# Kernel tuning notes

Measured on AMD Instinct MI355X. Metric: run time of the kernel, lower is better.

## Reference

```python
import jax, jax.numpy as jnp
import numpy as np

H = 768          # hidden_size
NH = 12          # num heads
HD = H // NH     # head dim = 64
FF = 4 * H       # 3072
EPS = 1e-12


def _layer_norm(x, g, b):
    mu = jnp.mean(x, axis=-1, keepdims=True)
    var = jnp.var(x, axis=-1, keepdims=True)
    return (x - mu) * jax.lax.rsqrt(var + EPS) * g + b


def setup_inputs() -> dict:
    key = jax.random.key(0)
    ks = jax.random.split(key, 8)
    B, S = 4, 2048
    s = 0.02
    return {
        "x": jax.random.normal(ks[0], (B, S, H), dtype=jnp.float32),
        "w_qkv": jax.random.normal(ks[1], (H, 3 * H), dtype=jnp.float32) * s,
        "b_qkv": jnp.zeros((3 * H,), dtype=jnp.float32),
        "w_out": jax.random.normal(ks[2], (H, H), dtype=jnp.float32) * s,
        "b_out": jnp.zeros((H,), dtype=jnp.float32),
        "w_ff1": jax.random.normal(ks[3], (H, FF), dtype=jnp.float32) * s,
        "b_ff1": jnp.zeros((FF,), dtype=jnp.float32),
        "w_ff2": jax.random.normal(ks[4], (FF, H), dtype=jnp.float32) * s,
        "b_ff2": jnp.zeros((H,), dtype=jnp.float32),
        "g1": jnp.ones((H,), dtype=jnp.float32),
        "be1": jnp.zeros((H,), dtype=jnp.float32),
        "g2": jnp.ones((H,), dtype=jnp.float32),
        "be2": jnp.zeros((H,), dtype=jnp.float32),
    }


def reference(x, w_qkv, b_qkv, w_out, b_out, w_ff1, b_ff1, w_ff2, b_ff2, g1, be1, g2, be2):
    B, S, _ = x.shape
    qkv = x @ w_qkv + b_qkv                     # [B,S,3H]
    q, k, v = jnp.split(qkv, 3, axis=-1)
    # [B,S,H] -> [B,NH,S,HD]
    def heads(t):
        return t.reshape(B, S, NH, HD).transpose(0, 2, 1, 3)
    q, k, v = heads(q), heads(k), heads(v)
    scores = jnp.einsum("bhqd,bhkd->bhqk", q, k) / np.sqrt(HD).astype(np.float32)
    attn = jax.nn.softmax(scores, axis=-1)      # dropout is identity at inference
    ctx = jnp.einsum("bhqk,bhkd->bhqd", attn, v)
    ctx = ctx.transpose(0, 2, 1, 3).reshape(B, S, H)
    attn_out = ctx @ w_out + b_out
    x1 = _layer_norm(x + attn_out, g1, be1)
    h = jax.nn.gelu(x1 @ w_ff1 + b_ff1, approximate=False)  # torch exact gelu
    ffn = h @ w_ff2 + b_ff2
    return _layer_norm(x1 + ffn, g2, be2)
```

## Files before the change

### kernel.cpp

```cpp
#include <hip/hip_runtime.h>
#include <cstdint>
#include <cstddef>

typedef unsigned short u16;
typedef __attribute__((ext_vector_type(8))) short bf16x8;
typedef __attribute__((ext_vector_type(4))) float f32x4;
typedef __attribute__((ext_vector_type(16))) float f32x16;

__device__ __forceinline__ u16 f2b(float f) {
    union { float f; unsigned u; } un; un.f = f;
    unsigned r = un.u + 0x7fffu + ((un.u >> 16) & 1u);
    return (u16)(r >> 16);
}
__device__ __forceinline__ u16 f2b_trunc(float f) {
    union { float f; unsigned u; } un; un.f = f;
    return (u16)(un.u >> 16);
}
__device__ __forceinline__ float b2f(u16 h) {
    union { unsigned u; float f; } un; un.u = ((unsigned)h) << 16;
    return un.f;
}
__device__ __forceinline__ float fast_exp2(float x) {
#if __has_builtin(__builtin_amdgcn_exp2f)
    return __builtin_amdgcn_exp2f(x);
#else
    return exp2f(x);
#endif
}

__device__ __forceinline__ void stage16(const u16* g, u16* l) {
    __builtin_amdgcn_global_load_lds(
        (const __attribute__((address_space(1))) void*)g,
        (__attribute__((address_space(3))) void*)l, 16, 0, 0);
}

__global__ __launch_bounds__(256)
void prep(const float* __restrict__ x, u16* __restrict__ xb,
          const float* __restrict__ wqkv, u16* __restrict__ wqkvT,
          const float* __restrict__ wout, u16* __restrict__ woutT,
          const float* __restrict__ wff1, u16* __restrict__ wff1T,
          const float* __restrict__ wff2, u16* __restrict__ wff2T) {
    __shared__ float t[32][33];
    const int tid = threadIdx.x;
    int bid = blockIdx.x;
    if (bid < 6144) {
        const int i = bid * 256 + tid;
        float4 v = ((const float4*)x)[i];
        ushort4 o;
        o.x = f2b(v.x); o.y = f2b(v.y); o.z = f2b(v.z); o.w = f2b(v.w);
        ((ushort4*)xb)[i] = o;
        return;
    }
    int tt = bid - 6144;
    const float* in; u16* out; int K, N, bx, by;
    if (tt < 1728)      { in = wqkv; out = wqkvT; K = 768;  N = 2304; bx = tt % 72; by = tt / 72; }
    else if ((tt -= 1728) < 576)  { in = wout; out = woutT; K = 768;  N = 768;  bx = tt % 24; by = tt / 24; }
    else if ((tt -= 576) < 2304)  { in = wff1; out = wff1T; K = 768;  N = 3072; bx = tt % 96; by = tt / 96; }
    else { tt -= 2304;    in = wff2; out = wff2T; K = 3072; N = 768;  bx = tt % 24; by = tt / 24; }
    const int n0 = bx * 32, k0 = by * 32;
    const int tx = tid & 31, ty = tid >> 5;
#pragma unroll
    for (int i = 0; i < 4; ++i)
        t[ty + i * 8][tx] = in[(size_t)(k0 + ty + i * 8) * N + n0 + tx];
    __syncthreads();
#pragma unroll
    for (int i = 0; i < 4; ++i)
        out[(size_t)(n0 + ty + i * 8) * K + k0 + tx] = f2b(t[tx][ty + i * 8]);
}

template <int EPI>
__global__ __launch_bounds__(256, 3)
void gemm_bf16(const u16* __restrict__ A, const u16* __restrict__ BT,
               const float* __restrict__ bias,
               void* __restrict__ outp, u16* __restrict__ vt, int M, int N, int K) {
    __shared__ __align__(16) u16 Ash[128 * 64];
    __shared__ __align__(16) u16 Bsh[128 * 64];
    const int m0 = blockIdx.y * 128, n0 = blockIdx.x * 128;
    const int tid = threadIdx.x;
    const int w = tid >> 6, lane = tid & 63;
    const int l32 = lane & 31, half = lane >> 5;
    const int wm = (w >> 1) * 64, wn = (w & 1) * 64;

    const int srow = lane >> 3;
    const int sgrp = (lane & 7) ^ (srow & 7);
    const int xr = l32 & 7;

    f32x16 acc[2][2];
#pragma unroll
    for (int i = 0; i < 2; ++i)
#pragma unroll
        for (int j = 0; j < 2; ++j)
#pragma unroll
            for (int e = 0; e < 16; ++e) acc[i][j][e] = 0.f;

    for (int k0 = 0; k0 < K; k0 += 64) {
#pragma unroll
        for (int it = 0; it < 4; ++it) {
            const int c = it * 4 + w;
            const int r = c * 8 + srow;
            stage16(A + (size_t)(m0 + r) * K + k0 + sgrp * 8, &Ash[c * 512 + lane * 8]);
        }
#pragma unroll
        for (int it = 0; it < 4; ++it) {
            const int c = it * 4 + w;
            const int r = c * 8 + srow;
            stage16(BT + (size_t)(n0 + r) * K + k0 + sgrp * 8, &Bsh[c * 512 + lane * 8]);
        }
        __syncthreads();

        bf16x8 af[2][4], bfr[2][4];
#pragma unroll
        for (int mt = 0; mt < 2; ++mt)
#pragma unroll
            for (int kc = 0; kc < 4; ++kc)
                af[mt][kc] = *(const bf16x8*)&Ash[(wm + mt * 32 + l32) * 64 +
                                                  (((kc << 1) + half) ^ xr) * 8];
#pragma unroll
        for (int nt = 0; nt < 2; ++nt)
#pragma unroll
            for (int kc = 0; kc < 4; ++kc)
                bfr[nt][kc] = *(const bf16x8*)&Bsh[(wn + nt * 32 + l32) * 64 +
                                                   (((kc << 1) + half) ^ xr) * 8];
#pragma unroll
        for (int mt = 0; mt < 2; ++mt)
#pragma unroll
            for (int nt = 0; nt < 2; ++nt)
#pragma unroll
                for (int kc = 0; kc < 4; ++kc)
                    acc[mt][nt] = __builtin_amdgcn_mfma_f32_32x32x16_bf16(
                        af[mt][kc], bfr[nt][kc], acc[mt][nt], 0, 0, 0);
        __syncthreads();
    }

    if (EPI == 3 && n0 >= 1536) {
#pragma unroll
        for (int mt = 0; mt < 2; ++mt) {
#pragma unroll
            for (int nt = 0; nt < 2; ++nt) {
                const int col = n0 + wn + nt * 32 + l32;
                const int c = col - 1536;
                const int h = c >> 6, d = c & 63;
                const float bv = bias[col];
#pragma unroll
                for (int rq = 0; rq < 4; ++rq) {
                    const int row0 = m0 + wm + mt * 32 + rq * 8 + half * 4;
                    const int b = row0 >> 11, tok = row0 & 2047;
                    ushort4 o;
                    o.x = f2b(acc[mt][nt][rq * 4 + 0] + bv);
                    o.y = f2b(acc[mt][nt][rq * 4 + 1] + bv);
                    o.z = f2b(acc[mt][nt][rq * 4 + 2] + bv);
                    o.w = f2b(acc[mt][nt][rq * 4 + 3] + bv);
                    *(ushort4*)&vt[(size_t)(((b * 12 + h) << 6) + d) * 2048 + tok] = o;
                }
            }
        }
        return;
    }

#pragma unroll
    for (int mt = 0; mt < 2; ++mt) {
#pragma unroll
        for (int nt = 0; nt < 2; ++nt) {
            const int col = n0 + wn + nt * 32 + l32;
            const float bv = bias[col];
#pragma unroll
            for (int reg = 0; reg < 16; ++reg) {
                const int row = m0 + wm + mt * 32 + (reg & 3) + 8 * (reg >> 2) + 4 * half;
                float v = acc[mt][nt][reg] + bv;
                if (EPI == 2)
                    v = 0.5f * v * (1.f + erff(v * 0.70710678118654752f));
                ((u16*)outp)[(size_t)row * N + col] = f2b(v);
            }
        }
    }
}

template <bool RESF32>
__global__ __launch_bounds__(256, 4)
void gemm_bf16_r64(const u16* __restrict__ A, const u16* __restrict__ BT,
                   const float* __restrict__ bias, const void* __restrict__ resid,
                   u16* __restrict__ outp, int M, int N, int K) {
    __shared__ __align__(16) u16 Ash[64 * 64];
    __shared__ __align__(16) u16 Bsh[128 * 64];
    const int m0 = blockIdx.y * 64, n0 = blockIdx.x * 128;
    const int tid = threadIdx.x;
    const int w = tid >> 6, lane = tid & 63;
    const int l32 = lane & 31, half = lane >> 5;
    const int wm = (w >> 1) * 32, wn = (w & 1) * 64;

    const int srow = lane >> 3;
    const int sgrp = (lane & 7) ^ (srow & 7);
    const int xr = l32 & 7;

    f32x16 acc[2];
#pragma unroll
    for (int j = 0; j < 2; ++j)
#pragma unroll
        for (int e = 0; e < 16; ++e) acc[j][e] = 0.f;

    for (int k0 = 0; k0 < K; k0 += 64) {
#pragma unroll
        for (int it = 0; it < 2; ++it) {
            const int c = it * 4 + w;
            const int r = c * 8 + srow;
            stage16(A + (size_t)(m0 + r) * K + k0 + sgrp * 8, &Ash[c * 512 + lane * 8]);
        }
#pragma unroll
        for (int it = 0; it < 4; ++it) {
            const int c = it * 4 + w;
            const int r = c * 8 + srow;
            stage16(BT + (size_t)(n0 + r) * K + k0 + sgrp * 8, &Bsh[c * 512 + lane * 8]);
        }
        __syncthreads();

        bf16x8 af[4], bfr[2][4];
#pragma unroll
        for (int kc = 0; kc < 4; ++kc)
            af[kc] = *(const bf16x8*)&Ash[(wm + l32) * 64 + (((kc << 1) + half) ^ xr) * 8];
#pragma unroll
        for (int nt = 0; nt < 2; ++nt)
#pragma unroll
            for (int kc = 0; kc < 4; ++kc)
                bfr[nt][kc] = *(const bf16x8*)&Bsh[(wn + nt * 32 + l32) * 64 +
                                                   (((kc << 1) + half) ^ xr) * 8];
#pragma unroll
        for (int nt = 0; nt < 2; ++nt)
#pragma unroll
            for (int kc = 0; kc < 4; ++kc)
                acc[nt] = __builtin_amdgcn_mfma_f32_32x32x16_bf16(
                    af[kc], bfr[nt][kc], acc[nt], 0, 0, 0);
        __syncthreads();
    }

#pragma unroll
    for (int nt = 0; nt < 2; ++nt) {
        const int col = n0 + wn + nt * 32 + l32;
        const float bv = bias[col];
#pragma unroll
        for (int reg = 0; reg < 16; ++reg) {
            const int row = m0 + wm + (reg & 3) + 8 * (reg >> 2) + 4 * half;
            const size_t idx = (size_t)row * N + col;
            const float rv = RESF32 ? ((const float*)resid)[idx]
                                    : b2f(((const u16*)resid)[idx]);
            outp[idx] = f2b(acc[nt][reg] + bv + rv);
        }
    }
}

__global__ __launch_bounds__(256, 2)
void attn_fused(const u16* __restrict__ qkv, const u16* __restrict__ vt,
                u16* __restrict__ ctx) {
    constexpr int LDP = 68;
    __shared__ __align__(16) u16 Ksh[64 * 64];
    __shared__ __align__(16) u16 Vsh[64 * 64];
    __shared__ __align__(16) short Psh[4 * 32 * LDP];

    const int q0 = blockIdx.x * 128;
    const int h = blockIdx.y, b = blockIdx.z;
    const int tid = threadIdx.x;
    const int w = tid >> 6, lane = tid & 63, l16 = lane & 15, quad = lane >> 4;
    short* Pw = Psh + w * 32 * LDP;

    const int srow = lane >> 3;
    const int sgrp = (lane & 7) ^ (srow & 7);
    const int xk = l16 & 7;

    const u16* Qp = qkv + (size_t)b * 2048 * 2304 + h * 64;
    const u16* Kp = Qp + 768;
    const u16* Vtp = vt + ((size_t)(b * 12 + h) << 6) * 2048;

    bf16x8 qf[2][2];
#pragma unroll
    for (int mt = 0; mt < 2; ++mt)
#pragma unroll
        for (int s = 0; s < 2; ++s)
            qf[mt][s] = *(const bf16x8*)(Qp +
                (size_t)(q0 + w * 32 + mt * 16 + l16) * 2304 + s * 32 + quad * 8);

    const f32x4 vzero = {0.f, 0.f, 0.f, 0.f};
    f32x4 oacc[2][4];
    float l_r[2][4];
#pragma unroll
    for (int mt = 0; mt < 2; ++mt) {
#pragma unroll
        for (int dt = 0; dt < 4; ++dt) oacc[mt][dt] = vzero;
#pragma unroll
        for (int r = 0; r < 4; ++r) l_r[mt][r] = 0.f;
    }

    constexpr float SCALE = 0.18033688011112042f;

    for (int kt = 0; kt < 2048; kt += 64) {
#pragma unroll
        for (int it = 0; it < 2; ++it) {
            const int c = it * 4 + w;
            const int r = c * 8 + srow;
            stage16(Kp + (size_t)(kt + r) * 2304 + sgrp * 8, &Ksh[c * 512 + lane * 8]);
        }
#pragma unroll
        for (int it = 0; it < 2; ++it) {
            const int c = it * 4 + w;
            const int r = c * 8 + srow;
            stage16(Vtp + (size_t)r * 2048 + kt + sgrp * 8, &Vsh[c * 512 + lane * 8]);
        }
        __syncthreads();

        bf16x8 kfr[4][2];
#pragma unroll
        for (int nt = 0; nt < 4; ++nt)
#pragma unroll
            for (int s = 0; s < 2; ++s)
                kfr[nt][s] = *(const bf16x8*)&Ksh[(nt * 16 + l16) * 64 +
                                                  (((s << 2) + quad) ^ xk) * 8];

        f32x4 sacc[2][4];
#pragma unroll
        for (int mt = 0; mt < 2; ++mt)
#pragma unroll
            for (int nt = 0; nt < 4; ++nt) {
                sacc[mt][nt] = vzero;
#pragma unroll
                for (int s = 0; s < 2; ++s)
                    sacc[mt][nt] = __builtin_amdgcn_mfma_f32_16x16x32_bf16(
                        qf[mt][s], kfr[nt][s], sacc[mt][nt], 0, 0, 0);
            }

#pragma unroll
        for (int mt = 0; mt < 2; ++mt) {
#pragma unroll
            for (int r = 0; r < 4; ++r) {
                float p0 = fast_exp2(sacc[mt][0][r] * SCALE);
                float p1 = fast_exp2(sacc[mt][1][r] * SCALE);
                float p2 = fast_exp2(sacc[mt][2][r] * SCALE);
                float p3 = fast_exp2(sacc[mt][3][r] * SCALE);
                l_r[mt][r] += (p0 + p1) + (p2 + p3);
                short* prow = &Pw[(mt * 16 + quad * 4 + r) * LDP + l16];
                prow[0]  = (short)f2b_trunc(p0);
                prow[16] = (short)f2b_trunc(p1);
                prow[32] = (short)f2b_trunc(p2);
                prow[48] = (short)f2b_trunc(p3);
            }
        }

        bf16x8 vfr[4][2];
#pragma unroll
        for (int dt = 0; dt < 4; ++dt)
#pragma unroll
            for (int s = 0; s < 2; ++s)
                vfr[dt][s] = *(const bf16x8*)&Vsh[(dt * 16 + l16) * 64 +
                                                  (((s << 2) + quad) ^ xk) * 8];

#pragma unroll
        for (int mt = 0; mt < 2; ++mt) {
            bf16x8 pf[2];
#pragma unroll
            for (int s = 0; s < 2; ++s) {
                union { struct { short4 lo, hi; } h2; bf16x8 v; } u;
                const short* base = &Pw[(mt * 16 + l16) * LDP + s * 32 + quad * 8];
                u.h2.lo = *(const short4*)(base);
                u.h2.hi = *(const short4*)(base + 4);
                pf[s] = u.v;
            }
#pragma unroll
            for (int dt = 0; dt < 4; ++dt)
#pragma unroll
                for (int s = 0; s < 2; ++s)
                    oacc[mt][dt] = __builtin_amdgcn_mfma_f32_16x16x32_bf16(
                        pf[s], vfr[dt][s], oacc[mt][dt], 0, 0, 0);
        }
        __syncthreads();
    }

#pragma unroll
    for (int mt = 0; mt < 2; ++mt)
#pragma unroll
        for (int r = 0; r < 4; ++r) {
#pragma unroll
            for (int off = 1; off < 16; off <<= 1)
                l_r[mt][r] += __shfl_xor(l_r[mt][r], off);
            l_r[mt][r] = 1.f / l_r[mt][r];
        }

#pragma unroll
    for (int mt = 0; mt < 2; ++mt)
#pragma unroll
        for (int dt = 0; dt < 4; ++dt)
#pragma unroll
            for (int r = 0; r < 4; ++r) {
                const int row = q0 + w * 32 + mt * 16 + quad * 4 + r;
                ctx[(size_t)(b * 2048 + row) * 768 + h * 64 + dt * 16 + l16] =
                    f2b(oacc[mt][dt][r] * l_r[mt][r]);
            }
}

template <bool OUTF32>
__global__ __launch_bounds__(256)
void layernorm_k(const u16* __restrict__ y, const float* __restrict__ g,
                 const float* __restrict__ be, float* __restrict__ outf,
                 u16* __restrict__ outb) {
    const int row = blockIdx.x;
    const int tid = threadIdx.x;
    const u16* yr = y + (size_t)row * 768;
    float v[3], s = 0.f, s2 = 0.f;
#pragma unroll
    for (int i = 0; i < 3; ++i) {
        float x = b2f(yr[tid + i * 256]);
        v[i] = x; s += x; s2 += x * x;
    }
#pragma unroll
    for (int off = 32; off >= 1; off >>= 1) {
        s += __shfl_xor(s, off);
        s2 += __shfl_xor(s2, off);
    }
    __shared__ float red[2][4];
    const int w = tid >> 6;
    if ((tid & 63) == 0) { red[0][w] = s; red[1][w] = s2; }
    __syncthreads();
    s = red[0][0] + red[0][1] + red[0][2] + red[0][3];
    s2 = red[1][0] + red[1][1] + red[1][2] + red[1][3];
    const float mu = s * (1.f / 768.f);
    const float var = s2 * (1.f / 768.f) - mu * mu;
    const float rs = rsqrtf(var + 1e-12f);
#pragma unroll
    for (int i = 0; i < 3; ++i) {
        const int c = tid + i * 256;
        const float o = (v[i] - mu) * rs * g[c] + be[c];
        if (OUTF32) outf[(size_t)row * 768 + c] = o;
        else        outb[(size_t)row * 768 + c] = f2b(o);
    }
}

extern "C" void kernel_launch(void* const* d_in, const int* in_sizes, int n_in,
                              void* d_out, int out_size, void* d_ws, size_t ws_size,
                              hipStream_t stream) {
    const float* x    = (const float*)d_in[0];
    const float* wqkv = (const float*)d_in[1];
    const float* bqkv = (const float*)d_in[2];
    const float* wout = (const float*)d_in[3];
    const float* bout = (const float*)d_in[4];
    const float* wff1 = (const float*)d_in[5];
    const float* bff1 = (const float*)d_in[6];
    const float* wff2 = (const float*)d_in[7];
    const float* bff2 = (const float*)d_in[8];
    const float* g1   = (const float*)d_in[9];
    const float* be1  = (const float*)d_in[10];
    const float* g2   = (const float*)d_in[11];
    const float* be2  = (const float*)d_in[12];

    char* ws = (char*)d_ws;
    constexpr size_t o_xb    = 0;
    constexpr size_t o_wqkvT = o_xb    + (size_t)8192 * 768 * 2;
    constexpr size_t o_woutT = o_wqkvT + (size_t)2304 * 768 * 2;
    constexpr size_t o_wff1T = o_woutT + (size_t)768 * 768 * 2;
    constexpr size_t o_wff2T = o_wff1T + (size_t)3072 * 768 * 2;
    constexpr size_t o_qkv   = o_wff2T + (size_t)768 * 3072 * 2;
    constexpr size_t o_ctx   = o_qkv   + (size_t)8192 * 2304 * 2;
    constexpr size_t o_y     = o_ctx   + (size_t)8192 * 768 * 2;
    constexpr size_t o_x1b   = o_y     + (size_t)8192 * 768 * 2;
    constexpr size_t o_vt    = o_x1b;
    constexpr size_t o_h     = o_qkv;

    u16*   xb    = (u16*)(ws + o_xb);
    u16*   wqkvT = (u16*)(ws + o_wqkvT);
    u16*   woutT = (u16*)(ws + o_woutT);
    u16*   wff1T = (u16*)(ws + o_wff1T);
    u16*   wff2T = (u16*)(ws + o_wff2T);
    u16*   qkvb  = (u16*)(ws + o_qkv);
    u16*   ctxb  = (u16*)(ws + o_ctx);
    u16*   yb    = (u16*)(ws + o_y);
    u16*   x1b   = (u16*)(ws + o_x1b);
    u16*   hb    = (u16*)(ws + o_h);
    u16*   vt    = (u16*)(ws + o_vt);

    prep<<<13056, 256, 0, stream>>>(x, xb, wqkv, wqkvT, wout, woutT,
                                    wff1, wff1T, wff2, wff2T);

    gemm_bf16<3><<<dim3(2304 / 128, 8192 / 128), 256, 0, stream>>>(
        xb, wqkvT, bqkv, qkvb, vt, 8192, 2304, 768);

    attn_fused<<<dim3(2048 / 128, 12, 4), 256, 0, stream>>>(qkvb, vt, ctxb);

    gemm_bf16_r64<true><<<dim3(768 / 128, 8192 / 64), 256, 0, stream>>>(
        ctxb, woutT, bout, x, yb, 8192, 768, 768);

    layernorm_k<false><<<8192, 256, 0, stream>>>(yb, g1, be1, nullptr, x1b);

    gemm_bf16<2><<<dim3(3072 / 128, 8192 / 128), 256, 0, stream>>>(
        x1b, wff1T, bff1, hb, nullptr, 8192, 3072, 768);

    gemm_bf16_r64<false><<<dim3(768 / 128, 8192 / 64), 256, 0, stream>>>(
        hb, wff2T, bff2, x1b, yb, 8192, 768, 3072);

    layernorm_k<true><<<8192, 256, 0, stream>>>(yb, g2, be2, (float*)d_out, nullptr);
}
```

Baseline: 395.2 us.

## Widen QKV GEMM tile to 192 columns, approximate GELU, raise attention occupancy

The QKV projection GEMM now uses 128x192 tiles (three 32-wide n-subtiles per wave) with a kc-outer MFMA loop that loads B fragments on the fly. This reduces the block count and reuses each A tile across more columns. The FF1 epilogue swaps exact erf GELU for a tanh-style exp2/rcp approximation, which is cheaper but slightly less accurate than torch's exact gelu. Attention launch bounds are raised to 3 blocks per CU, which may force register spills.

```diff
diff --git a/kernel.cpp b/kernel.cpp
--- a/kernel.cpp
+++ b/kernel.cpp
@@ -26,6 +26,17 @@
 #else
     return exp2f(x);
 #endif
+}
+__device__ __forceinline__ float fast_rcp(float x) {
+#if __has_builtin(__builtin_amdgcn_rcpf)
+    return __builtin_amdgcn_rcpf(x);
+#else
+    return 1.f / x;
+#endif
+}
+__device__ __forceinline__ float gelu_fast(float v) {
+    const float s = fast_exp2(v * (2.30220842f + 0.10294324f * (v * v)));
+    return v - v * fast_rcp(s + 1.f);
 }
 
 __device__ __forceinline__ void stage16(const u16* g, u16* l) {
@@ -68,28 +79,28 @@
         out[(size_t)(n0 + ty + i * 8) * K + k0 + tx] = f2b(t[tx][ty + i * 8]);
 }
 
-template <int EPI>
+template <int EPI, int NTW>
 __global__ __launch_bounds__(256, 3)
 void gemm_bf16(const u16* __restrict__ A, const u16* __restrict__ BT,
                const float* __restrict__ bias,
                void* __restrict__ outp, u16* __restrict__ vt, int M, int N, int K) {
     __shared__ __align__(16) u16 Ash[128 * 64];
-    __shared__ __align__(16) u16 Bsh[128 * 64];
-    const int m0 = blockIdx.y * 128, n0 = blockIdx.x * 128;
+    __shared__ __align__(16) u16 Bsh[NTW * 64 * 64];
+    const int m0 = blockIdx.y * 128, n0 = blockIdx.x * (NTW * 64);
     const int tid = threadIdx.x;
     const int w = tid >> 6, lane = tid & 63;
     const int l32 = lane & 31, half = lane >> 5;
-    const int wm = (w >> 1) * 64, wn = (w & 1) * 64;
+    const int wm = (w >> 1) * 64, wn = (w & 1) * (NTW * 32);
 
     const int srow = lane >> 3;
     const int sgrp = (lane & 7) ^ (srow & 7);
     const int xr = l32 & 7;
 
-    f32x16 acc[2][2];
+    f32x16 acc[2][NTW];
 #pragma unroll
     for (int i = 0; i < 2; ++i)
 #pragma unroll
-        for (int j = 0; j < 2; ++j)
+        for (int j = 0; j < NTW; ++j)
 #pragma unroll
             for (int e = 0; e < 16; ++e) acc[i][j][e] = 0.f;
 
@@ -101,34 +112,51 @@
             stage16(A + (size_t)(m0 + r) * K + k0 + sgrp * 8, &Ash[c * 512 + lane * 8]);
         }
 #pragma unroll
-        for (int it = 0; it < 4; ++it) {
+        for (int it = 0; it < 2 * NTW; ++it) {
             const int c = it * 4 + w;
             const int r = c * 8 + srow;
             stage16(BT + (size_t)(n0 + r) * K + k0 + sgrp * 8, &Bsh[c * 512 + lane * 8]);
         }
         __syncthreads();
 
-        bf16x8 af[2][4], bfr[2][4];
-#pragma unroll
-        for (int mt = 0; mt < 2; ++mt)
-#pragma unroll
-            for (int kc = 0; kc < 4; ++kc)
-                af[mt][kc] = *(const bf16x8*)&Ash[(wm + mt * 32 + l32) * 64 +
-                                                  (((kc << 1) + half) ^ xr) * 8];
-#pragma unroll
-        for (int nt = 0; nt < 2; ++nt)
-#pragma unroll
-            for (int kc = 0; kc < 4; ++kc)
-                bfr[nt][kc] = *(const bf16x8*)&Bsh[(wn + nt * 32 + l32) * 64 +
-                                                   (((kc << 1) + half) ^ xr) * 8];
-#pragma unroll
-        for (int mt = 0; mt < 2; ++mt)
+        if constexpr (NTW == 2) {
+            bf16x8 af[2][4], bfr[2][4];
+#pragma unroll
+            for (int mt = 0; mt < 2; ++mt)
+#pragma unroll
+                for (int kc = 0; kc < 4; ++kc)
+                    af[mt][kc] = *(const bf16x8*)&Ash[(wm + mt * 32 + l32) * 64 +
+                                                      (((kc << 1) + half) ^ xr) * 8];
 #pragma unroll
             for (int nt = 0; nt < 2; ++nt)
 #pragma unroll
                 for (int kc = 0; kc < 4; ++kc)
-                    acc[mt][nt] = __builtin_amdgcn_mfma_f32_32x32x16_bf16(
-                        af[mt][kc], bfr[nt][kc], acc[mt][nt], 0, 0, 0);
+                    bfr[nt][kc] = *(const bf16x8*)&Bsh[(wn + nt * 32 + l32) * 64 +
+                                                       (((kc << 1) + half) ^ xr) * 8];
+#pragma unroll
+            for (int mt = 0; mt < 2; ++mt)
+#pragma unroll
+                for (int nt = 0; nt < 2; ++nt)
+#pragma unroll
+                    for (int kc = 0; kc < 4; ++kc)
+                        acc[mt][nt] = __builtin_amdgcn_mfma_f32_32x32x16_bf16(
+                            af[mt][kc], bfr[nt][kc], acc[mt][nt], 0, 0, 0);
+        } else {
+#pragma unroll
+            for (int kc = 0; kc < 4; ++kc) {
+                const int ko = (((kc << 1) + half) ^ xr) * 8;
+                bf16x8 a0 = *(const bf16x8*)&Ash[(wm + l32) * 64 + ko];
+                bf16x8 a1 = *(const bf16x8*)&Ash[(wm + 32 + l32) * 64 + ko];
+#pragma unroll
+                for (int nt = 0; nt < NTW; ++nt) {
+                    bf16x8 bv = *(const bf16x8*)&Bsh[(wn + nt * 32 + l32) * 64 + ko];
+                    acc[0][nt] = __builtin_amdgcn_mfma_f32_32x32x16_bf16(
+                        a0, bv, acc[0][nt], 0, 0, 0);
+                    acc[1][nt] = __builtin_amdgcn_mfma_f32_32x32x16_bf16(
+                        a1, bv, acc[1][nt], 0, 0, 0);
+                }
+            }
+        }
         __syncthreads();
     }
 
@@ -136,7 +164,7 @@
 #pragma unroll
         for (int mt = 0; mt < 2; ++mt) {
 #pragma unroll
-            for (int nt = 0; nt < 2; ++nt) {
+            for (int nt = 0; nt < NTW; ++nt) {
                 const int col = n0 + wn + nt * 32 + l32;
                 const int c = col - 1536;
                 const int h = c >> 6, d = c & 63;
@@ -160,7 +188,7 @@
 #pragma unroll
     for (int mt = 0; mt < 2; ++mt) {
 #pragma unroll
-        for (int nt = 0; nt < 2; ++nt) {
+        for (int nt = 0; nt < NTW; ++nt) {
             const int col = n0 + wn + nt * 32 + l32;
             const float bv = bias[col];
 #pragma unroll
@@ -168,7 +196,7 @@
                 const int row = m0 + wm + mt * 32 + (reg & 3) + 8 * (reg >> 2) + 4 * half;
                 float v = acc[mt][nt][reg] + bv;
                 if (EPI == 2)
-                    v = 0.5f * v * (1.f + erff(v * 0.70710678118654752f));
+                    v = gelu_fast(v);
                 ((u16*)outp)[(size_t)row * N + col] = f2b(v);
             }
         }
@@ -247,7 +275,7 @@
     }
 }
 
-__global__ __launch_bounds__(256, 2)
+__global__ __launch_bounds__(256, 3)
 void attn_fused(const u16* __restrict__ qkv, const u16* __restrict__ vt,
                 u16* __restrict__ ctx) {
     constexpr int LDP = 68;
@@ -475,7 +503,7 @@
     prep<<<13056, 256, 0, stream>>>(x, xb, wqkv, wqkvT, wout, woutT,
                                     wff1, wff1T, wff2, wff2T);
 
-    gemm_bf16<3><<<dim3(2304 / 128, 8192 / 128), 256, 0, stream>>>(
+    gemm_bf16<3, 3><<<dim3(2304 / 192, 8192 / 128), 256, 0, stream>>>(
         xb, wqkvT, bqkv, qkvb, vt, 8192, 2304, 768);
 
     attn_fused<<<dim3(2048 / 128, 12, 4), 256, 0, stream>>>(qkvb, vt, ctxb);
@@ -485,7 +513,7 @@
 
     layernorm_k<false><<<8192, 256, 0, stream>>>(yb, g1, be1, nullptr, x1b);
 
-    gemm_bf16<2><<<dim3(3072 / 128, 8192 / 128), 256, 0, stream>>>(
+    gemm_bf16<2, 2><<<dim3(3072 / 128, 8192 / 128), 256, 0, stream>>>(
         x1b, wff1T, bff1, hb, nullptr, 8192, 3072, 768);
 
     gemm_bf16_r64<false><<<dim3(768 / 128, 8192 / 64), 256, 0, stream>>>(
```

Measured after the change: 387.8 us. Within noise of the previous version (-1.9%).
